# Optimization experiments

Hardware: AMD Instinct MI355X
Metric: run time of the kernel (lower is better)

Reference implementation:

```python
import jax, jax.numpy as jnp
import numpy as np

STRIDE, PAD, DIL, KH, KW = 1, 1, 1, 3, 3

def conv2d(x, w, b):
    y = jax.lax.conv_general_dilated(x, w, window_strides=(STRIDE, STRIDE),
                                     padding=((PAD, PAD), (PAD, PAD)),
                                     rhs_dilation=(DIL, DIL),
                                     dimension_numbers=('NCHW', 'OIHW', 'NCHW'))
    return y + b[None, :, None, None]

def deform_conv2d(x, offset, mask, weight):
    # x: [B,C,H,W]; offset: [B,2*KK,Ho,Wo] (y,x interleaved per kernel point);
    # mask: [B,KK,Ho,Wo]; weight: [O,C,KH,KW]
    B, C, H, W = x.shape
    O = weight.shape[0]
    KK = KH * KW
    Ho, Wo = offset.shape[2], offset.shape[3]
    off = offset.reshape(B, KK, 2, Ho, Wo)
    dy, dx = off[:, :, 0], off[:, :, 1]
    ki, kj = jnp.meshgrid(jnp.arange(KH), jnp.arange(KW), indexing='ij')
    ki = ki.reshape(KK).astype(x.dtype)
    kj = kj.reshape(KK).astype(x.dtype)
    base_y = (jnp.arange(Ho) * STRIDE - PAD).astype(x.dtype)
    base_x = (jnp.arange(Wo) * STRIDE - PAD).astype(x.dtype)
    yy = base_y[None, None, :, None] + ki[None, :, None, None] * DIL + dy  # [B,KK,Ho,Wo]
    xx = base_x[None, None, None, :] + kj[None, :, None, None] * DIL + dx

    def sample(img, ys, xs):  # img [C,H,W]; ys/xs [KK,Ho,Wo]
        y0f = jnp.floor(ys); x0f = jnp.floor(xs)
        wy = ys - y0f; wx = xs - x0f
        y0 = y0f.astype(jnp.int32); x0 = x0f.astype(jnp.int32)
        def gather(yi, xi):
            valid = (yi >= 0) & (yi < H) & (xi >= 0) & (xi < W)
            yc = jnp.clip(yi, 0, H - 1); xc = jnp.clip(xi, 0, W - 1)
            return img[:, yc, xc] * valid[None].astype(img.dtype)  # [C,KK,Ho,Wo]
        v00 = gather(y0, x0); v01 = gather(y0, x0 + 1)
        v10 = gather(y0 + 1, x0); v11 = gather(y0 + 1, x0 + 1)
        return (v00 * (1 - wy) * (1 - wx) + v01 * (1 - wy) * wx
                + v10 * wy * (1 - wx) + v11 * wy * wx)

    patches = jax.vmap(sample)(x, yy, xx)          # [B,C,KK,Ho,Wo]
    patches = patches * mask[:, None]              # modulation
    return jnp.einsum('bckhw,ock->bohw', patches, weight.reshape(O, C, KK))

def setup_inputs() -> dict:
    key = jax.random.key(0)
    ks = jax.random.split(key, 6)
    B, Cin, Cout, H, W = 8, 64, 64, 128, 128
    KK = KH * KW
    x = jax.random.normal(ks[0], (B, Cin, H, W), dtype=jnp.float32)
    # Note: original zero-inits offset/modulator convs; we use small random
    # weights so the deformable sampling path is nontrivially exercised.
    offset_w = jax.random.normal(ks[1], (2 * KK, Cin, KH, KW), dtype=jnp.float32) * 0.02
    offset_b = jax.random.normal(ks[2], (2 * KK,), dtype=jnp.float32) * 0.1
    mod_w = jax.random.normal(ks[3], (KK, Cin, KH, KW), dtype=jnp.float32) * 0.02
    mod_b = jax.random.normal(ks[4], (KK,), dtype=jnp.float32) * 0.1
    weight = jax.random.normal(ks[5], (Cout, Cin, KH, KW), dtype=jnp.float32) * (1.0 / np.sqrt(Cin * KK))
    return {"x": x, "offset_w": offset_w, "offset_b": offset_b,
            "mod_w": mod_w, "mod_b": mod_b, "weight": weight}

def reference(x, offset_w, offset_b, mod_w, mod_b, weight):
    offset = conv2d(x, offset_w, offset_b)                 # [B,2*KK,Ho,Wo]
    modulator = 2.0 * jax.nn.sigmoid(conv2d(x, mod_w, mod_b))  # [B,KK,Ho,Wo]
    return deform_conv2d(x, offset, modulator, weight)
```

## Files before the change

kernel.cpp:

```cpp
#include <hip/hip_runtime.h>
#include <math.h>

#define B_   8
#define C_   64
#define O_   64
#define H_   128
#define W_   128
#define HW_  (H_ * W_)
#define KSZ  576

typedef _Float16 f16x8 __attribute__((ext_vector_type(8)));
typedef float    f32x4 __attribute__((ext_vector_type(4)));

#define WPM_BYTES (18 * 4 * 64 * 8 * 2)
#define WPA_BYTES (18 * 2 * 64 * 8 * 2)
#define TB2_      (B_ * HW_ / 128)

__global__ __launch_bounds__(256) void prep_kernel(
    const float* __restrict__ x,
    const float* __restrict__ offw, const float* __restrict__ modw,
    const float* __restrict__ wgt,
    _Float16* __restrict__ xT, _Float16* __restrict__ wpM, _Float16* __restrict__ wpA)
{
    const int bi = blockIdx.x;
    if (bi < TB2_) {
        __shared__ _Float16 tile[128 * 68];
        const int tid = threadIdx.x;
        const int b      = bi >> 7;
        const int pxbase = (bi & 127) * 128;

        const int px4   = (tid & 31) * 4;
        const int cbase = tid >> 5;
        const float* __restrict__ xp = x + (size_t)b * C_ * HW_ + pxbase;
#pragma unroll
        for (int r = 0; r < 8; ++r) {
            const int c = cbase + r * 8;
            const f32x4 v = *(const f32x4*)&xp[(size_t)c * HW_ + px4];
#pragma unroll
            for (int i = 0; i < 4; ++i)
                tile[(px4 + i) * 68 + c] = (_Float16)v[i];
        }
        __syncthreads();

        const int px = tid >> 1;
        const int c0 = (tid & 1) * 32;
        f16x8 w[4];
#pragma unroll
        for (int q = 0; q < 4; ++q)
#pragma unroll
            for (int j = 0; j < 8; ++j)
                w[q][j] = tile[px * 68 + c0 + q * 8 + j];
        _Float16* __restrict__ op = xT + ((size_t)b * HW_ + pxbase + px) * 64 + c0;
#pragma unroll
        for (int q = 0; q < 4; ++q)
            *(f16x8*)&op[q * 8] = w[q];
        return;
    }
    const int g = (bi - TB2_) * 256 + threadIdx.x;
    if (g < 18 * 4 * 64) {
        const int s = g >> 8, mt = (g >> 6) & 3, lane = g & 63;
        const int k = s >> 1, cb = (s & 1) * 32;
        const int o  = mt * 16 + (lane & 15);
        const int c0 = cb + (lane >> 4) * 8;
        f16x8 v;
#pragma unroll
        for (int j = 0; j < 8; ++j) v[j] = (_Float16)wgt[o * KSZ + (c0 + j) * 9 + k];
        *(f16x8*)&wpM[(size_t)g * 8] = v;
    } else if (g < 18 * 4 * 64 + 18 * 2 * 64) {
        const int u = g - 18 * 4 * 64;
        const int s = u >> 7, mt = (u >> 6) & 1, lane = u & 63;
        const int k = s >> 1, cb = (s & 1) * 32;
        const int t  = mt * 16 + (lane & 15);
        const int c0 = cb + (lane >> 4) * 8;
        f16x8 v;
#pragma unroll
        for (int j = 0; j < 8; ++j) {
            float w = 0.0f;
            if (t < 18)      w = offw[t * KSZ + (c0 + j) * 9 + k];
            else if (t < 27) w = modw[(t - 18) * KSZ + (c0 + j) * 9 + k];
            v[j] = (_Float16)w;
        }
        *(f16x8*)&wpA[(size_t)u * 8] = v;
    }
}

__device__ __forceinline__ f16x8 splat8(_Float16 h) {
    f16x8 v = {h, h, h, h, h, h, h, h};
    return v;
}

#define WROWS 11
#define WCOLS 22

__global__ __launch_bounds__(256) void dcn_main_kernel(
    const _Float16* __restrict__ xT,
    const _Float16* __restrict__ wpA,
    const _Float16* __restrict__ wpM,
    const float* __restrict__ offb,
    const float* __restrict__ modb,
    float* __restrict__ out)
{
    __shared__ _Float16 win[WROWS * WCOLS * 64];
    __shared__ float params[4][16][28];

    const int tid  = threadIdx.x;
    const int lane = tid & 63;
    const int wave = tid >> 6;
    const int lq   = lane >> 4;
    const int ln   = lane & 15;

    const int bi   = blockIdx.x;
    const int b    = bi & 7;
    const int rest = bi >> 3;
    const int ho   = (rest >> 3) * 4;
    const int x0b  = (rest & 7) * 16;

    const int wrow = wave;
    const int yo   = ho + wrow;
    const int pxw  = ln;
    const int wo   = x0b + pxw;

    const _Float16* __restrict__ xbT = xT + (size_t)b * HW_ * 64;

#pragma unroll
    for (int it = 0; it < 8; ++it) {
        const int e = it * 256 + tid;
        if (e < WROWS * WCOLS * 8) {
            const int r   = e / (WCOLS * 8);
            const int rem = e - r * (WCOLS * 8);
            const int cx  = rem >> 3;
            const int q   = rem & 7;
            const int yr  = ho - 3 + r;
            const int xc  = x0b - 3 + cx;
            f16x8 v = splat8((_Float16)0.0f);
            if (((unsigned)yr < H_) && ((unsigned)xc < W_))
                v = *(const f16x8*)&xbT[((size_t)(yr * W_ + xc)) * 64 + q * 8];
            *(f16x8*)&win[(r * WCOLS + cx) * 64 + ((q ^ (cx & 7)) * 8)] = v;
        }
    }
    __syncthreads();

    f32x4 accA[2];
#pragma unroll
    for (int mt = 0; mt < 2; ++mt) accA[mt] = (f32x4){0.f, 0.f, 0.f, 0.f};

#pragma unroll
    for (int s = 0; s < 18; ++s) {
        const int k = s >> 1, h = s & 1;
        const int ki = k / 3, kj = k - ki * 3;
        f16x8 afA[2];
#pragma unroll
        for (int mt = 0; mt < 2; ++mt)
            afA[mt] = *(const f16x8*)&wpA[(size_t)((s * 2 + mt) * 64 + lane) * 8];
        const int sy = wrow + ki + 2;
        const int sx = pxw + kj + 2;
        const int chunk = h * 4 + lq;
        const f16x8 bfA = *(const f16x8*)&win[(sy * WCOLS + sx) * 64 + ((chunk ^ (sx & 7)) * 8)];
#pragma unroll
        for (int mt = 0; mt < 2; ++mt)
            accA[mt] = __builtin_amdgcn_mfma_f32_16x16x32_f16(afA[mt], bfA, accA[mt], 0, 0, 0);
    }

#pragma unroll
    for (int mt = 0; mt < 2; ++mt)
#pragma unroll
        for (int r = 0; r < 4; ++r) {
            const int t = mt * 16 + lq * 4 + r;
            const float val = accA[mt][r];
            if (t < 18)      params[wrow][ln][t] = val + offb[t];
            else if (t < 27) params[wrow][ln][t] = 2.0f / (1.0f + expf(-(val + modb[t - 18])));
        }

    f32x4 acc[4];
#pragma unroll
    for (int mt = 0; mt < 4; ++mt) acc[mt] = (f32x4){0.f, 0.f, 0.f, 0.f};

#pragma unroll
    for (int k = 0; k < 9; ++k) {
        const int ki = k / 3, kj = k - ki * 3;

        const float dy = params[wrow][ln][2 * k];
        const float dx = params[wrow][ln][2 * k + 1];
        const float mk = params[wrow][ln][18 + k];

        const float ys = (float)(yo - 1 + ki) + dy;
        const float xs = (float)(wo - 1 + kj) + dx;
        const float y0f = floorf(ys), x0f = floorf(xs);
        const float wy = ys - y0f, wx = xs - x0f;
        const int y0 = (int)y0f, x0 = (int)x0f;
        const float wyc = 1.0f - wy, wxc = 1.0f - wx;
        const float w00 = wyc * wxc * mk;
        const float w01 = wyc * wx  * mk;
        const float w10 = wy  * wxc * mk;
        const float w11 = wy  * wx  * mk;

        const int sy0 = y0 - ho + 3, sy1 = sy0 + 1;
        const int sx0 = x0 - x0b + 3, sx1 = sx0 + 1;
        const int ok00 = ((unsigned)sy0 < WROWS) & ((unsigned)sx0 < WCOLS);
        const int ok01 = ((unsigned)sy0 < WROWS) & ((unsigned)sx1 < WCOLS);
        const int ok10 = ((unsigned)sy1 < WROWS) & ((unsigned)sx0 < WCOLS);
        const int ok11 = ((unsigned)sy1 < WROWS) & ((unsigned)sx1 < WCOLS);
        const int okk  = ok00 | (ok01 << 1) | (ok10 << 2) | (ok11 << 3);
        const int cy0 = min(max(sy0, 0), WROWS - 1), cy1 = min(max(sy1, 0), WROWS - 1);
        const int cx0 = min(max(sx0, 0), WCOLS - 1), cx1 = min(max(sx1, 0), WCOLS - 1);
        const int b00 = (cy0 * WCOLS + cx0) * 64, x7_00 = cx0 & 7;
        const int b01 = (cy0 * WCOLS + cx1) * 64, x7_01 = cx1 & 7;
        const int b10 = (cy1 * WCOLS + cx0) * 64, x7_10 = cx0 & 7;
        const int b11 = (cy1 * WCOLS + cx1) * 64, x7_11 = cx1 & 7;

        const f16x8 w00v = splat8((_Float16)w00);
        const f16x8 w01v = splat8((_Float16)w01);
        const f16x8 w10v = splat8((_Float16)w10);
        const f16x8 w11v = splat8((_Float16)w11);

#pragma unroll
        for (int h = 0; h < 2; ++h) {
            const int s = 2 * k + h;
            const int chunk = h * 4 + lq;
            const int c0 = h * 32 + lq * 8;

            f16x8 af[4];
#pragma unroll
            for (int mt = 0; mt < 4; ++mt)
                af[mt] = *(const f16x8*)&wpM[(size_t)((s * 4 + mt) * 64 + lane) * 8];

            f16x8 a00 = *(const f16x8*)&win[b00 + ((chunk ^ x7_00) * 8)];
            f16x8 a01 = *(const f16x8*)&win[b01 + ((chunk ^ x7_01) * 8)];
            f16x8 a10 = *(const f16x8*)&win[b10 + ((chunk ^ x7_10) * 8)];
            f16x8 a11 = *(const f16x8*)&win[b11 + ((chunk ^ x7_11) * 8)];

            if (__builtin_expect(okk != 15, 0)) {
                if (!ok00) {
                    const int yc = min(max(y0, 0), H_ - 1), xc = min(max(x0, 0), W_ - 1);
                    const bool in = ((unsigned)y0 < H_) && ((unsigned)x0 < W_);
                    a00 = in ? *(const f16x8*)&xbT[((size_t)(yc * W_ + xc)) * 64 + c0] : splat8((_Float16)0.0f);
                }
                if (!ok01) {
                    const int yc = min(max(y0, 0), H_ - 1), xc = min(max(x0 + 1, 0), W_ - 1);
                    const bool in = ((unsigned)y0 < H_) && ((unsigned)(x0 + 1) < W_);
                    a01 = in ? *(const f16x8*)&xbT[((size_t)(yc * W_ + xc)) * 64 + c0] : splat8((_Float16)0.0f);
                }
                if (!ok10) {
                    const int yc = min(max(y0 + 1, 0), H_ - 1), xc = min(max(x0, 0), W_ - 1);
                    const bool in = ((unsigned)(y0 + 1) < H_) && ((unsigned)x0 < W_);
                    a10 = in ? *(const f16x8*)&xbT[((size_t)(yc * W_ + xc)) * 64 + c0] : splat8((_Float16)0.0f);
                }
                if (!ok11) {
                    const int yc = min(max(y0 + 1, 0), H_ - 1), xc = min(max(x0 + 1, 0), W_ - 1);
                    const bool in = ((unsigned)(y0 + 1) < H_) && ((unsigned)(x0 + 1) < W_);
                    a11 = in ? *(const f16x8*)&xbT[((size_t)(yc * W_ + xc)) * 64 + c0] : splat8((_Float16)0.0f);
                }
            }

            f16x8 r = a00 * w00v;
            r = a01 * w01v + r;
            r = a10 * w10v + r;
            r = a11 * w11v + r;

#pragma unroll
            for (int mt = 0; mt < 4; ++mt)
                acc[mt] = __builtin_amdgcn_mfma_f32_16x16x32_f16(af[mt], r, acc[mt], 0, 0, 0);
        }
    }

    float* __restrict__ ob = out + (size_t)b * O_ * HW_ + (size_t)yo * W_;
#pragma unroll
    for (int mt = 0; mt < 4; ++mt)
#pragma unroll
        for (int r = 0; r < 4; ++r) {
            const int o = mt * 16 + lq * 4 + r;
            ob[(size_t)o * HW_ + wo] = acc[mt][r];
        }
}

extern "C" void kernel_launch(void* const* d_in, const int* in_sizes, int n_in,
                              void* d_out, int out_size, void* d_ws, size_t ws_size,
                              hipStream_t stream) {
    (void)in_sizes; (void)n_in; (void)out_size; (void)ws_size;
    const float* x    = (const float*)d_in[0];
    const float* offw = (const float*)d_in[1];
    const float* offb = (const float*)d_in[2];
    const float* modw = (const float*)d_in[3];
    const float* modb = (const float*)d_in[4];
    const float* wgt  = (const float*)d_in[5];
    float* out = (float*)d_out;

    _Float16* wpM = (_Float16*)d_ws;
    _Float16* wpA = (_Float16*)((char*)d_ws + WPM_BYTES);
    _Float16* xT  = (_Float16*)((char*)d_ws + WPM_BYTES + WPA_BYTES);

    prep_kernel<<<TB2_ + 27, 256, 0, stream>>>(x, offw, modw, wgt, xT, wpM, wpA);
    dcn_main_kernel<<<B_ * H_ * 2, 256, 0, stream>>>(xT, wpA, wpM, offb, modb, out);
}
```

Before: 133.7 us.

## Software-pipeline deformable tap sampling to prefetch next tap's LDS gathers

```diff
diff --git a/kernel.cpp b/kernel.cpp
--- a/kernel.cpp
+++ b/kernel.cpp
@@ -175,93 +175,120 @@
 #pragma unroll
     for (int mt = 0; mt < 4; ++mt) acc[mt] = (f32x4){0.f, 0.f, 0.f, 0.f};
 
-#pragma unroll
-    for (int k = 0; k < 9; ++k) {
-        const int ki = k / 3, kj = k - ki * 3;
-
-        const float dy = params[wrow][ln][2 * k];
-        const float dx = params[wrow][ln][2 * k + 1];
-        const float mk = params[wrow][ln][18 + k];
-
-        const float ys = (float)(yo - 1 + ki) + dy;
-        const float xs = (float)(wo - 1 + kj) + dx;
-        const float y0f = floorf(ys), x0f = floorf(xs);
-        const float wy = ys - y0f, wx = xs - x0f;
-        const int y0 = (int)y0f, x0 = (int)x0f;
-        const float wyc = 1.0f - wy, wxc = 1.0f - wx;
-        const float w00 = wyc * wxc * mk;
-        const float w01 = wyc * wx  * mk;
-        const float w10 = wy  * wxc * mk;
-        const float w11 = wy  * wx  * mk;
-
-        const int sy0 = y0 - ho + 3, sy1 = sy0 + 1;
-        const int sx0 = x0 - x0b + 3, sx1 = sx0 + 1;
-        const int ok00 = ((unsigned)sy0 < WROWS) & ((unsigned)sx0 < WCOLS);
-        const int ok01 = ((unsigned)sy0 < WROWS) & ((unsigned)sx1 < WCOLS);
-        const int ok10 = ((unsigned)sy1 < WROWS) & ((unsigned)sx0 < WCOLS);
-        const int ok11 = ((unsigned)sy1 < WROWS) & ((unsigned)sx1 < WCOLS);
-        const int okk  = ok00 | (ok01 << 1) | (ok10 << 2) | (ok11 << 3);
-        const int cy0 = min(max(sy0, 0), WROWS - 1), cy1 = min(max(sy1, 0), WROWS - 1);
-        const int cx0 = min(max(sx0, 0), WCOLS - 1), cx1 = min(max(sx1, 0), WCOLS - 1);
-        const int b00 = (cy0 * WCOLS + cx0) * 64, x7_00 = cx0 & 7;
-        const int b01 = (cy0 * WCOLS + cx1) * 64, x7_01 = cx1 & 7;
-        const int b10 = (cy1 * WCOLS + cx0) * 64, x7_10 = cx0 & 7;
-        const int b11 = (cy1 * WCOLS + cx1) * 64, x7_11 = cx1 & 7;
-
-        const f16x8 w00v = splat8((_Float16)w00);
-        const f16x8 w01v = splat8((_Float16)w01);
-        const f16x8 w10v = splat8((_Float16)w10);
-        const f16x8 w11v = splat8((_Float16)w11);
-
-#pragma unroll
-        for (int h = 0; h < 2; ++h) {
-            const int s = 2 * k + h;
-            const int chunk = h * 4 + lq;
-            const int c0 = h * 32 + lq * 8;
-
-            f16x8 af[4];
-#pragma unroll
-            for (int mt = 0; mt < 4; ++mt)
-                af[mt] = *(const f16x8*)&wpM[(size_t)((s * 4 + mt) * 64 + lane) * 8];
-
-            f16x8 a00 = *(const f16x8*)&win[b00 + ((chunk ^ x7_00) * 8)];
-            f16x8 a01 = *(const f16x8*)&win[b01 + ((chunk ^ x7_01) * 8)];
-            f16x8 a10 = *(const f16x8*)&win[b10 + ((chunk ^ x7_10) * 8)];
-            f16x8 a11 = *(const f16x8*)&win[b11 + ((chunk ^ x7_11) * 8)];
-
-            if (__builtin_expect(okk != 15, 0)) {
-                if (!ok00) {
-                    const int yc = min(max(y0, 0), H_ - 1), xc = min(max(x0, 0), W_ - 1);
-                    const bool in = ((unsigned)y0 < H_) && ((unsigned)x0 < W_);
-                    a00 = in ? *(const f16x8*)&xbT[((size_t)(yc * W_ + xc)) * 64 + c0] : splat8((_Float16)0.0f);
-                }
-                if (!ok01) {
-                    const int yc = min(max(y0, 0), H_ - 1), xc = min(max(x0 + 1, 0), W_ - 1);
-                    const bool in = ((unsigned)y0 < H_) && ((unsigned)(x0 + 1) < W_);
-                    a01 = in ? *(const f16x8*)&xbT[((size_t)(yc * W_ + xc)) * 64 + c0] : splat8((_Float16)0.0f);
-                }
-                if (!ok10) {
-                    const int yc = min(max(y0 + 1, 0), H_ - 1), xc = min(max(x0, 0), W_ - 1);
-                    const bool in = ((unsigned)(y0 + 1) < H_) && ((unsigned)x0 < W_);
-                    a10 = in ? *(const f16x8*)&xbT[((size_t)(yc * W_ + xc)) * 64 + c0] : splat8((_Float16)0.0f);
-                }
-                if (!ok11) {
-                    const int yc = min(max(y0 + 1, 0), H_ - 1), xc = min(max(x0 + 1, 0), W_ - 1);
-                    const bool in = ((unsigned)(y0 + 1) < H_) && ((unsigned)(x0 + 1) < W_);
-                    a11 = in ? *(const f16x8*)&xbT[((size_t)(yc * W_ + xc)) * 64 + c0] : splat8((_Float16)0.0f);
-                }
-            }
-
-            f16x8 r = a00 * w00v;
-            r = a01 * w01v + r;
-            r = a10 * w10v + r;
-            r = a11 * w11v + r;
-
-#pragma unroll
-            for (int mt = 0; mt < 4; ++mt)
-                acc[mt] = __builtin_amdgcn_mfma_f32_16x16x32_f16(af[mt], r, acc[mt], 0, 0, 0);
-        }
-    }
+    f16x8 pa[2][4];
+    int   pe[2][4];
+    float pw[2][4];
+    int   pok[2], py0[2], px0[2];
+
+#define FIXC(av, bv, yy, xx) do {                                             \
+        const int yc_ = min(max((yy), 0), H_ - 1);                            \
+        const int xc_ = min(max((xx), 0), W_ - 1);                            \
+        const bool in_ = ((unsigned)(yy) < H_) && ((unsigned)(xx) < W_);      \
+        const _Float16* fp_ = &xbT[((size_t)(yc_ * W_ + xc_)) * 64 + lq * 8]; \
+        (av) = in_ ? *(const f16x8*)&fp_[0]  : splat8((_Float16)0.0f);        \
+        (bv) = in_ ? *(const f16x8*)&fp_[32] : splat8((_Float16)0.0f);        \
+    } while (0)
+
+#define TAPSTAGE(kk, par) do {                                                \
+        const int ki_ = (kk) / 3, kj_ = (kk) - ki_ * 3;                       \
+        const float dy_ = params[wrow][ln][2 * (kk)];                         \
+        const float dx_ = params[wrow][ln][2 * (kk) + 1];                     \
+        const float mk_ = params[wrow][ln][18 + (kk)];                        \
+        const float ys_ = (float)(yo - 1 + ki_) + dy_;                        \
+        const float xs_ = (float)(wo - 1 + kj_) + dx_;                        \
+        const float y0f_ = floorf(ys_), x0f_ = floorf(xs_);                   \
+        const float wy_ = ys_ - y0f_, wx_ = xs_ - x0f_;                       \
+        const int y0_ = (int)y0f_, x0_ = (int)x0f_;                           \
+        const float wyc_ = 1.0f - wy_, wxc_ = 1.0f - wx_;                     \
+        pw[par][0] = wyc_ * wxc_ * mk_;                                       \
+        pw[par][1] = wyc_ * wx_  * mk_;                                       \
+        pw[par][2] = wy_  * wxc_ * mk_;                                       \
+        pw[par][3] = wy_  * wx_  * mk_;                                       \
+        const int sy0_ = y0_ - ho + 3, sy1_ = sy0_ + 1;                       \
+        const int sx0_ = x0_ - x0b + 3, sx1_ = sx0_ + 1;                      \
+        const int o00_ = ((unsigned)sy0_ < WROWS) & ((unsigned)sx0_ < WCOLS); \
+        const int o01_ = ((unsigned)sy0_ < WROWS) & ((unsigned)sx1_ < WCOLS); \
+        const int o10_ = ((unsigned)sy1_ < WROWS) & ((unsigned)sx0_ < WCOLS); \
+        const int o11_ = ((unsigned)sy1_ < WROWS) & ((unsigned)sx1_ < WCOLS); \
+        pok[par] = o00_ | (o01_ << 1) | (o10_ << 2) | (o11_ << 3);            \
+        py0[par] = y0_; px0[par] = x0_;                                       \
+        const int cy0_ = min(max(sy0_, 0), WROWS - 1);                        \
+        const int cy1_ = min(max(sy1_, 0), WROWS - 1);                        \
+        const int cx0_ = min(max(sx0_, 0), WCOLS - 1);                        \
+        const int cx1_ = min(max(sx1_, 0), WCOLS - 1);                        \
+        const int x70_ = cx0_ & 7, x71_ = cx1_ & 7;                           \
+        pe[par][0] = (cy0_ * WCOLS + cx0_) * 64 + ((lq ^ x70_) * 8);          \
+        pe[par][1] = (cy0_ * WCOLS + cx1_) * 64 + ((lq ^ x71_) * 8);          \
+        pe[par][2] = (cy1_ * WCOLS + cx0_) * 64 + ((lq ^ x70_) * 8);          \
+        pe[par][3] = (cy1_ * WCOLS + cx1_) * 64 + ((lq ^ x71_) * 8);          \
+        pa[par][0] = *(const f16x8*)&win[pe[par][0]];                         \
+        pa[par][1] = *(const f16x8*)&win[pe[par][1]];                         \
+        pa[par][2] = *(const f16x8*)&win[pe[par][2]];                         \
+        pa[par][3] = *(const f16x8*)&win[pe[par][3]];                         \
+    } while (0)
+
+#define CONSUME(kk, par) do {                                                 \
+        f16x8 b0_ = *(const f16x8*)&win[pe[par][0] ^ 32];                     \
+        f16x8 b1_ = *(const f16x8*)&win[pe[par][1] ^ 32];                     \
+        f16x8 b2_ = *(const f16x8*)&win[pe[par][2] ^ 32];                     \
+        f16x8 b3_ = *(const f16x8*)&win[pe[par][3] ^ 32];                     \
+        f16x8 a0_ = pa[par][0], a1_ = pa[par][1];                             \
+        f16x8 a2_ = pa[par][2], a3_ = pa[par][3];                             \
+        const int okk_ = pok[par];                                            \
+        if (__builtin_expect(okk_ != 15, 0)) {                                \
+            const int y0_ = py0[par], x0_ = px0[par];                         \
+            if (!(okk_ & 1)) FIXC(a0_, b0_, y0_,     x0_);                    \
+            if (!(okk_ & 2)) FIXC(a1_, b1_, y0_,     x0_ + 1);                \
+            if (!(okk_ & 4)) FIXC(a2_, b2_, y0_ + 1, x0_);                    \
+            if (!(okk_ & 8)) FIXC(a3_, b3_, y0_ + 1, x0_ + 1);                \
+        }                                                                     \
+        const f16x8 w0_ = splat8((_Float16)pw[par][0]);                       \
+        const f16x8 w1_ = splat8((_Float16)pw[par][1]);                       \
+        const f16x8 w2_ = splat8((_Float16)pw[par][2]);                       \
+        const f16x8 w3_ = splat8((_Float16)pw[par][3]);                       \
+        {                                                                     \
+            const int s_ = 2 * (kk);                                          \
+            f16x8 af0_ = *(const f16x8*)&wpM[(size_t)((s_ * 4 + 0) * 64 + lane) * 8]; \
+            f16x8 af1_ = *(const f16x8*)&wpM[(size_t)((s_ * 4 + 1) * 64 + lane) * 8]; \
+            f16x8 af2_ = *(const f16x8*)&wpM[(size_t)((s_ * 4 + 2) * 64 + lane) * 8]; \
+            f16x8 af3_ = *(const f16x8*)&wpM[(size_t)((s_ * 4 + 3) * 64 + lane) * 8]; \
+            f16x8 r_ = a0_ * w0_;                                             \
+            r_ = a1_ * w1_ + r_;                                              \
+            r_ = a2_ * w2_ + r_;                                              \
+            r_ = a3_ * w3_ + r_;                                              \
+            acc[0] = __builtin_amdgcn_mfma_f32_16x16x32_f16(af0_, r_, acc[0], 0, 0, 0); \
+            acc[1] = __builtin_amdgcn_mfma_f32_16x16x32_f16(af1_, r_, acc[1], 0, 0, 0); \
+            acc[2] = __builtin_amdgcn_mfma_f32_16x16x32_f16(af2_, r_, acc[2], 0, 0, 0); \
+            acc[3] = __builtin_amdgcn_mfma_f32_16x16x32_f16(af3_, r_, acc[3], 0, 0, 0); \
+        }                                                                     \
+        {                                                                     \
+            const int s_ = 2 * (kk) + 1;                                      \
+            f16x8 af0_ = *(const f16x8*)&wpM[(size_t)((s_ * 4 + 0) * 64 + lane) * 8]; \
+            f16x8 af1_ = *(const f16x8*)&wpM[(size_t)((s_ * 4 + 1) * 64 + lane) * 8]; \
+            f16x8 af2_ = *(const f16x8*)&wpM[(size_t)((s_ * 4 + 2) * 64 + lane) * 8]; \
+            f16x8 af3_ = *(const f16x8*)&wpM[(size_t)((s_ * 4 + 3) * 64 + lane) * 8]; \
+            f16x8 r_ = b0_ * w0_;                                             \
+            r_ = b1_ * w1_ + r_;                                              \
+            r_ = b2_ * w2_ + r_;                                              \
+            r_ = b3_ * w3_ + r_;                                              \
+            acc[0] = __builtin_amdgcn_mfma_f32_16x16x32_f16(af0_, r_, acc[0], 0, 0, 0); \
+            acc[1] = __builtin_amdgcn_mfma_f32_16x16x32_f16(af1_, r_, acc[1], 0, 0, 0); \
+            acc[2] = __builtin_amdgcn_mfma_f32_16x16x32_f16(af2_, r_, acc[2], 0, 0, 0); \
+            acc[3] = __builtin_amdgcn_mfma_f32_16x16x32_f16(af3_, r_, acc[3], 0, 0, 0); \
+        }                                                                     \
+    } while (0)
+
+    TAPSTAGE(0, 0);
+#pragma unroll
+    for (int k = 1; k < 9; ++k) {
+        if (k & 1) { TAPSTAGE(k, 1); CONSUME(k - 1, 0); }
+        else       { TAPSTAGE(k, 0); CONSUME(k - 1, 1); }
+    }
+    CONSUME(8, 0);
+
+#undef CONSUME
+#undef TAPSTAGE
+#undef FIXC
 
     float* __restrict__ ob = out + (size_t)b * O_ * HW_ + (size_t)yo * W_;
 #pragma unroll
```

New measurement: 133.4 us. No clear change (-0.2%).
